# Optimization experiments

Hardware: AMD Instinct MI355X
Metric: run time of the kernel (lower is better)

Reference implementation:

```python
import jax, jax.numpy as jnp
import numpy as np

EMBED_DIM = 1024
N_HEADS = 16
HEAD_DIM = EMBED_DIM // N_HEADS


def setup_inputs() -> dict:
    key = jax.random.key(0)
    k_x, k_wi, k_bi, k_wo, k_bo = jax.random.split(key, 5)
    B, N, C = 4, 2048, EMBED_DIM
    scale = 1.0 / np.sqrt(C)
    return {
        "x": jax.random.normal(k_x, (B, N, C), dtype=jnp.float32),
        "w_in": jax.random.normal(k_wi, (C, 3 * C), dtype=jnp.float32) * scale,
        "b_in": jax.random.normal(k_bi, (3 * C,), dtype=jnp.float32) * 0.01,
        "w_out": jax.random.normal(k_wo, (C, C), dtype=jnp.float32) * scale,
        "b_out": jax.random.normal(k_bo, (C,), dtype=jnp.float32) * 0.01,
    }


def reference(x, w_in, b_in, w_out, b_out):
    B, N, C = x.shape
    H, D = N_HEADS, HEAD_DIM
    qkv = x @ w_in + b_in  # (B, N, 3C)
    q, k, v = jnp.split(qkv, 3, axis=-1)
    # (B, H, N, D)
    q = q.reshape(B, N, H, D).transpose(0, 2, 1, 3)
    k = k.reshape(B, N, H, D).transpose(0, 2, 1, 3)
    v = v.reshape(B, N, H, D).transpose(0, 2, 1, 3)
    # Naive attention: full (B,H,N,N) scores, NO sqrt(d) scaling (as in source)
    scores = jnp.einsum("bhnd,bhmd->bhnm", q, k)
    attn = jax.nn.softmax(scores, axis=-1)
    out = jnp.einsum("bhnm,bhmd->bhnd", attn, v)
    out = out.transpose(0, 2, 1, 3).reshape(B, N, C)
    return out @ w_out + b_out
```

## Files before the change

kernel.cpp:

```cpp
#include <hip/hip_runtime.h>
#include <hip/hip_bf16.h>
#include <stdint.h>

typedef __attribute__((ext_vector_type(8))) __bf16 bf8v;
typedef __attribute__((ext_vector_type(4))) float f4v;

#define L2E 1.44269504088896f

__device__ __forceinline__ unsigned short f2bf(float f) {
  union { float f; unsigned u; } v; v.f = f;
  unsigned r = v.u + 0x7fffu + ((v.u >> 16) & 1u);
  return (unsigned short)(r >> 16);
}

__device__ __forceinline__ unsigned pk2bf(float f0, float f1) {
  union { __hip_bfloat162 h; unsigned u; } c;
  c.h = __float22bfloat162_rn(make_float2(f0, f1));
  return c.u;
}

__device__ __forceinline__ float exp2_hw(float x) {
  return __builtin_amdgcn_exp2f(x);
}

__device__ __forceinline__ void gl_lds16(const void* g, void* l) {
  __builtin_amdgcn_global_load_lds(
      (__attribute__((address_space(1))) void*)(g),
      (__attribute__((address_space(3))) void*)(l), 16, 0, 0);
}

__device__ __forceinline__ void store_out(unsigned short* p, float v) { *p = f2bf(v); }
__device__ __forceinline__ void store_out(float* p, float v) { *p = v; }

__global__ void prep_kernel(const float* __restrict__ x,
                            const float* __restrict__ w_in,
                            const float* __restrict__ w_out,
                            unsigned short* __restrict__ xb,
                            unsigned short* __restrict__ wiT,
                            unsigned short* __restrict__ woT) {
  __shared__ float tile[32][33];
  int bx = blockIdx.x;
  if (bx < 8192) {
    int i = bx * 256 + threadIdx.x;
    float4 v = ((const float4*)x)[i];
    ushort4 o;
    o.x = f2bf(v.x); o.y = f2bf(v.y); o.z = f2bf(v.z); o.w = f2bf(v.w);
    ((ushort4*)xb)[i] = o;
    return;
  }
  int idx = bx - 8192;
  int bxx = idx & 127, byy = idx >> 7;
  const float* in; unsigned short* out; int C, c0;
  if (bxx < 96) { in = w_in;  out = wiT; C = 3072; c0 = bxx * 32; }
  else          { in = w_out; out = woT; C = 1024; c0 = (bxx - 96) * 32; }
  int r0 = byy * 32;
  int tx = threadIdx.x & 31, ty = threadIdx.x >> 5;
#pragma unroll
  for (int j = 0; j < 4; ++j)
    tile[ty + 8 * j][tx] = in[(size_t)(r0 + ty + 8 * j) * C + c0 + tx];
  __syncthreads();
#pragma unroll
  for (int j = 0; j < 4; ++j)
    out[(size_t)(c0 + ty + 8 * j) * 1024 + r0 + tx] = f2bf(tile[tx][ty + 8 * j]);
}

__global__ void transpose_v_kernel(const unsigned short* __restrict__ qkv,
                                   unsigned short* __restrict__ vtg) {
  __shared__ unsigned short tile[32][33];
  int bh = blockIdx.z;
  int d0 = blockIdx.y * 32;
  int n0 = blockIdx.x * 32;
  int b = bh >> 4, h = bh & 15;
  int tx = threadIdx.x, ty = threadIdx.y;
  const unsigned short* src = qkv + (size_t)b * 2048 * 3072 + 2048 + h * 64 + d0;
#pragma unroll
  for (int j = 0; j < 4; ++j)
    tile[ty + 8 * j][tx] = src[(size_t)(n0 + ty + 8 * j) * 3072 + tx];
  __syncthreads();
  unsigned short* dst = vtg + ((size_t)bh * 64) * 2048;
#pragma unroll
  for (int j = 0; j < 4; ++j)
    dst[(size_t)(d0 + ty + 8 * j) * 2048 + n0 + tx] = tile[tx][ty + 8 * j];
}

template <typename OutT, bool SCALE>
__global__ __launch_bounds__(512, 2) void gemm256(
    const unsigned short* __restrict__ A,
    const unsigned short* __restrict__ BT,
    const float* __restrict__ bias,
    OutT* __restrict__ C,
    int N, int K, int nbx, int scale_ncols, float scale) {
  __shared__ __align__(16) unsigned short As[2][256 * 64];
  __shared__ __align__(16) unsigned short Bs[2][128 * 64];
  const int tid = threadIdx.x;
  const int wave = tid >> 6, lane = tid & 63;
  const int lo = lane & 15, hi = lane >> 4;
  const int wm = wave >> 1, wn = wave & 1;

  const int cpx = gridDim.x >> 3;
  const int s = (blockIdx.x & 7) * cpx + (blockIdx.x >> 3);
  const int by = s / nbx, bx = s - by * nbx;
  const int m0 = by * 256, n0 = bx * 128;

  const int srow = lane >> 3;
  const int scol = (((lane & 7) ^ (srow & 7)) * 8);
  const unsigned short* gA = A + (size_t)(m0 + wave * 8 + srow) * K + scol;
  const unsigned short* gB = BT + (size_t)(n0 + wave * 8 + srow) * K + scol;

  const int csw0 = ((hi ^ (lo & 7)) * 8);
  const int csw1 = (((4 + hi) ^ (lo & 7)) * 8);
  const int rA = wm * 64;
  const int rB = wn * 64;

  f4v acc[4][4] = {};
  const int nt = K >> 6;

#pragma unroll
  for (int j = 0; j < 4; ++j)
    gl_lds16(gA + (size_t)(j * 64) * K, &As[0][(j * 64 + wave * 8) * 64]);
#pragma unroll
  for (int j = 0; j < 2; ++j)
    gl_lds16(gB + (size_t)(j * 64) * K, &Bs[0][(j * 64 + wave * 8) * 64]);

  for (int t = 0; t < nt; ++t) {
    const int c = t & 1;
    __builtin_amdgcn_s_barrier();
    __builtin_amdgcn_sched_barrier(0);
    if (t + 1 < nt) {
      const unsigned short* gA1 = gA + (size_t)(t + 1) * 64;
      const unsigned short* gB1 = gB + (size_t)(t + 1) * 64;
#pragma unroll
      for (int j = 0; j < 4; ++j)
        gl_lds16(gA1 + (size_t)(j * 64) * K, &As[c ^ 1][(j * 64 + wave * 8) * 64]);
#pragma unroll
      for (int j = 0; j < 2; ++j)
        gl_lds16(gB1 + (size_t)(j * 64) * K, &Bs[c ^ 1][(j * 64 + wave * 8) * 64]);
      asm volatile("s_waitcnt vmcnt(6)" ::: "memory");
    } else {
      asm volatile("s_waitcnt vmcnt(0)" ::: "memory");
    }
    __builtin_amdgcn_sched_barrier(0);
    __builtin_amdgcn_s_barrier();
    __builtin_amdgcn_sched_barrier(0);

    bf8v b[4][2];
#pragma unroll
    for (int fn = 0; fn < 4; ++fn) {
      b[fn][0] = *(const bf8v*)&Bs[c][(rB + fn * 16 + lo) * 64 + csw0];
      b[fn][1] = *(const bf8v*)&Bs[c][(rB + fn * 16 + lo) * 64 + csw1];
    }
#pragma unroll
    for (int p = 0; p < 2; ++p) {
      bf8v a[2][2];
#pragma unroll
      for (int i = 0; i < 2; ++i) {
        a[i][0] = *(const bf8v*)&As[c][(rA + (p * 2 + i) * 16 + lo) * 64 + csw0];
        a[i][1] = *(const bf8v*)&As[c][(rA + (p * 2 + i) * 16 + lo) * 64 + csw1];
      }
      __builtin_amdgcn_s_setprio(1);
#pragma unroll
      for (int ks = 0; ks < 2; ++ks)
#pragma unroll
        for (int i = 0; i < 2; ++i)
#pragma unroll
          for (int fn = 0; fn < 4; ++fn)
            acc[p * 2 + i][fn] = __builtin_amdgcn_mfma_f32_16x16x32_bf16(
                a[i][ks], b[fn][ks], acc[p * 2 + i][fn], 0, 0, 0);
      __builtin_amdgcn_s_setprio(0);
    }
  }

#pragma unroll
  for (int i = 0; i < 4; ++i) {
#pragma unroll
    for (int r = 0; r < 4; ++r) {
      int row = m0 + wm * 64 + i * 16 + hi * 4 + r;
#pragma unroll
      for (int j = 0; j < 4; ++j) {
        int col = n0 + wn * 64 + j * 16 + lo;
        float v = acc[i][j][r] + bias[col];
        if (SCALE && col < scale_ncols) v *= scale;
        store_out(&C[(size_t)row * N + col], v);
      }
    }
  }
}

#define FSTR 72

__global__ __launch_bounds__(256, 2) void flash_attn(
    const unsigned short* __restrict__ qkv,
    const unsigned short* __restrict__ vtg,
    unsigned short* __restrict__ y) {
  __shared__ __align__(16) unsigned short Ps[256 * FSTR];
  __shared__ __align__(16) unsigned short Kt[2][64 * FSTR];
  __shared__ __align__(16) unsigned short Vt[2][64 * FSTR];
  const int tid = threadIdx.x;
  const int wave = tid >> 6, lane = tid & 63;
  const int lo = lane & 15, hi = lane >> 4;

  const int lin = blockIdx.x;
  const int swz = (lin & 7) * 64 + (lin >> 3);
  const int q0 = (swz & 7) << 8;
  const int h  = (swz >> 3) & 15;
  const int b  = swz >> 7;

  const size_t base = (size_t)b * 2048 * 3072;
  const int qoff = h * 64, koff = 1024 + h * 64;
  const unsigned short* vsrc = vtg + (size_t)(b * 16 + h) * 64 * 2048;

  const int m_st = tid >> 3, c_st = tid & 7;
  const unsigned short* kg = qkv + base + koff;
  float4 rk0, rk1, rv0, rv1;
  auto kv_load = [&](int kt) {
    const int mb = kt * 64;
    rk0 = *(const float4*)(kg + (size_t)(mb + m_st) * 3072 + c_st * 8);
    rk1 = *(const float4*)(kg + (size_t)(mb + m_st + 32) * 3072 + c_st * 8);
    rv0 = *(const float4*)(vsrc + (size_t)m_st * 2048 + mb + c_st * 8);
    rv1 = *(const float4*)(vsrc + (size_t)(m_st + 32) * 2048 + mb + c_st * 8);
  };
  auto kv_write = [&](int buf) {
    *(float4*)&Kt[buf][m_st * FSTR + c_st * 8] = rk0;
    *(float4*)&Kt[buf][(m_st + 32) * FSTR + c_st * 8] = rk1;
    *(float4*)&Vt[buf][m_st * FSTR + c_st * 8] = rv0;
    *(float4*)&Vt[buf][(m_st + 32) * FSTR + c_st * 8] = rv1;
  };

  kv_load(0);

#pragma unroll
  for (int i = 0; i < 8; ++i) {
    int cid = i * 256 + tid;
    int m = cid >> 3, c = cid & 7;
    *(float4*)&Ps[m * FSTR + c * 8] =
        *(const float4*)(qkv + base + (size_t)(q0 + m) * 3072 + qoff + c * 8);
  }
  __syncthreads();
  bf8v bq[4][2];
#pragma unroll
  for (int qt = 0; qt < 4; ++qt)
#pragma unroll
    for (int ks = 0; ks < 2; ++ks)
      bq[qt][ks] = *(const bf8v*)&Ps[(wave * 64 + qt * 16 + lo) * FSTR + ks * 32 + hi * 8];

  f4v O[4][4] = {};
  f4v acc_l[4] = {};
  union { bf8v v; unsigned short u[8]; } onesu;
#pragma unroll
  for (int i = 0; i < 8; ++i) onesu.u[i] = 0x3F80;
  const bf8v ones = onesu.v;

  kv_write(0);
  kv_load(1);
  asm volatile("s_waitcnt lgkmcnt(0)" ::: "memory");
  __builtin_amdgcn_s_barrier();
  asm volatile("" ::: "memory");

  for (int kt = 0; kt < 32; ++kt) {
    const int c = kt & 1;
    if (kt < 31) {
      kv_write(c ^ 1);
      if (kt < 30) kv_load(kt + 2);
    }

#pragma unroll
    for (int ct = 0; ct < 4; ++ct) {
      f4v s[4] = {{}, {}, {}, {}};
      __builtin_amdgcn_s_setprio(1);
#pragma unroll
      for (int ks = 0; ks < 2; ++ks) {
        bf8v ak = *(const bf8v*)&Kt[c][(ct * 16 + lo) * FSTR + ks * 32 + hi * 8];
#pragma unroll
        for (int qt = 0; qt < 4; ++qt)
          s[qt] = __builtin_amdgcn_mfma_f32_16x16x32_bf16(ak, bq[qt][ks], s[qt], 0, 0, 0);
      }
      __builtin_amdgcn_s_setprio(0);
#pragma unroll
      for (int qt = 0; qt < 4; ++qt) {
        float p0 = exp2_hw(s[qt][0]), p1 = exp2_hw(s[qt][1]);
        float p2 = exp2_hw(s[qt][2]), p3 = exp2_hw(s[qt][3]);
        uint2 w; w.x = pk2bf(p0, p1); w.y = pk2bf(p2, p3);
        *(uint2*)&Ps[(wave * 64 + qt * 16 + lo) * FSTR + ct * 16 + hi * 4] = w;
      }
    }

#pragma unroll
    for (int ks = 0; ks < 2; ++ks) {
      bf8v ap[4];
#pragma unroll
      for (int qt = 0; qt < 4; ++qt)
        ap[qt] = *(const bf8v*)&Ps[(wave * 64 + qt * 16 + lo) * FSTR + ks * 32 + hi * 8];
      __builtin_amdgcn_s_setprio(1);
#pragma unroll
      for (int qt = 0; qt < 4; ++qt)
        acc_l[qt] = __builtin_amdgcn_mfma_f32_16x16x32_bf16(ap[qt], ones, acc_l[qt], 0, 0, 0);
#pragma unroll
      for (int dt = 0; dt < 4; ++dt) {
        bf8v bv = *(const bf8v*)&Vt[c][(dt * 16 + lo) * FSTR + ks * 32 + hi * 8];
#pragma unroll
        for (int qt = 0; qt < 4; ++qt)
          O[qt][dt] = __builtin_amdgcn_mfma_f32_16x16x32_bf16(ap[qt], bv, O[qt][dt], 0, 0, 0);
      }
      __builtin_amdgcn_s_setprio(0);
    }

    asm volatile("s_waitcnt lgkmcnt(0)" ::: "memory");
    __builtin_amdgcn_s_barrier();
    asm volatile("" ::: "memory");
  }

#pragma unroll
  for (int qt = 0; qt < 4; ++qt) {
#pragma unroll
    for (int r = 0; r < 4; ++r) {
      float inv = 1.f / acc_l[qt][r];
      int row = q0 + wave * 64 + qt * 16 + hi * 4 + r;
      size_t orow = ((size_t)b * 2048 + row) * 1024 + h * 64;
#pragma unroll
      for (int dt = 0; dt < 4; ++dt)
        y[orow + dt * 16 + lo] = f2bf(O[qt][dt][r] * inv);
    }
  }
}

extern "C" void kernel_launch(void* const* d_in, const int* in_sizes, int n_in,
                              void* d_out, int out_size, void* d_ws, size_t ws_size,
                              hipStream_t stream) {
  (void)in_sizes; (void)n_in; (void)out_size; (void)ws_size;
  const float* x     = (const float*)d_in[0];
  const float* w_in  = (const float*)d_in[1];
  const float* b_in  = (const float*)d_in[2];
  const float* w_out = (const float*)d_in[3];
  const float* b_out = (const float*)d_in[4];

  unsigned short* xb  = (unsigned short*)d_ws;
  unsigned short* wiT = xb  + (size_t)8192 * 1024;
  unsigned short* woT = wiT + (size_t)3072 * 1024;
  unsigned short* qkv = woT + (size_t)1024 * 1024;
  unsigned short* yb  = qkv + (size_t)8192 * 3072;
  unsigned short* vtg = xb;

  prep_kernel<<<12288, 256, 0, stream>>>(x, w_in, w_out, xb, wiT, woT);

  gemm256<unsigned short, true><<<768, 512, 0, stream>>>(
      xb, wiT, b_in, qkv, 3072, 1024, 24, 1024, L2E);
  transpose_v_kernel<<<dim3(64, 2, 64), dim3(32, 8), 0, stream>>>(qkv, vtg);
  flash_attn<<<512, 256, 0, stream>>>(qkv, vtg, yb);
  gemm256<float, false><<<256, 512, 0, stream>>>(
      yb, woT, b_out, (float*)d_out, 1024, 1024, 8, 0, 1.0f);
}
```

Before: 278.6 us.

## Load K/V fragments directly from global memory, drop LDS staging and barriers

The flash attention kernel now has each wave read its K and V MFMA operand fragments straight from global memory into registers, instead of staging them cooperatively through double-buffered shared-memory tiles. Q fragments are also read directly. This removes the LDS K/V buffers and the per-iteration block barrier, so waves can run independently. In exchange, every wave redundantly fetches the full K/V tile (four times more global/L2 traffic), and the loads are no longer prefetched ahead, so memory latency is exposed inside the loop.

```diff
diff --git a/kernel.cpp b/kernel.cpp
--- a/kernel.cpp
+++ b/kernel.cpp
@@ -193,8 +193,6 @@
     const unsigned short* __restrict__ vtg,
     unsigned short* __restrict__ y) {
   __shared__ __align__(16) unsigned short Ps[256 * FSTR];
-  __shared__ __align__(16) unsigned short Kt[2][64 * FSTR];
-  __shared__ __align__(16) unsigned short Vt[2][64 * FSTR];
   const int tid = threadIdx.x;
   const int wave = tid >> 6, lane = tid & 63;
   const int lo = lane & 15, hi = lane >> 4;
@@ -208,40 +206,15 @@
   const size_t base = (size_t)b * 2048 * 3072;
   const int qoff = h * 64, koff = 1024 + h * 64;
   const unsigned short* vsrc = vtg + (size_t)(b * 16 + h) * 64 * 2048;
-
-  const int m_st = tid >> 3, c_st = tid & 7;
   const unsigned short* kg = qkv + base + koff;
-  float4 rk0, rk1, rv0, rv1;
-  auto kv_load = [&](int kt) {
-    const int mb = kt * 64;
-    rk0 = *(const float4*)(kg + (size_t)(mb + m_st) * 3072 + c_st * 8);
-    rk1 = *(const float4*)(kg + (size_t)(mb + m_st + 32) * 3072 + c_st * 8);
-    rv0 = *(const float4*)(vsrc + (size_t)m_st * 2048 + mb + c_st * 8);
-    rv1 = *(const float4*)(vsrc + (size_t)(m_st + 32) * 2048 + mb + c_st * 8);
-  };
-  auto kv_write = [&](int buf) {
-    *(float4*)&Kt[buf][m_st * FSTR + c_st * 8] = rk0;
-    *(float4*)&Kt[buf][(m_st + 32) * FSTR + c_st * 8] = rk1;
-    *(float4*)&Vt[buf][m_st * FSTR + c_st * 8] = rv0;
-    *(float4*)&Vt[buf][(m_st + 32) * FSTR + c_st * 8] = rv1;
-  };
-
-  kv_load(0);
-
-#pragma unroll
-  for (int i = 0; i < 8; ++i) {
-    int cid = i * 256 + tid;
-    int m = cid >> 3, c = cid & 7;
-    *(float4*)&Ps[m * FSTR + c * 8] =
-        *(const float4*)(qkv + base + (size_t)(q0 + m) * 3072 + qoff + c * 8);
-  }
-  __syncthreads();
+
   bf8v bq[4][2];
 #pragma unroll
   for (int qt = 0; qt < 4; ++qt)
 #pragma unroll
     for (int ks = 0; ks < 2; ++ks)
-      bq[qt][ks] = *(const bf8v*)&Ps[(wave * 64 + qt * 16 + lo) * FSTR + ks * 32 + hi * 8];
+      bq[qt][ks] = *(const bf8v*)(qkv + base +
+          (size_t)(q0 + wave * 64 + qt * 16 + lo) * 3072 + qoff + ks * 32 + hi * 8);
 
   f4v O[4][4] = {};
   f4v acc_l[4] = {};
@@ -250,37 +223,41 @@
   for (int i = 0; i < 8; ++i) onesu.u[i] = 0x3F80;
   const bf8v ones = onesu.v;
 
-  kv_write(0);
-  kv_load(1);
-  asm volatile("s_waitcnt lgkmcnt(0)" ::: "memory");
-  __builtin_amdgcn_s_barrier();
-  asm volatile("" ::: "memory");
+  const int prow = (wave * 64 + lo) * FSTR;
 
   for (int kt = 0; kt < 32; ++kt) {
-    const int c = kt & 1;
-    if (kt < 31) {
-      kv_write(c ^ 1);
-      if (kt < 30) kv_load(kt + 2);
-    }
+    const unsigned short* kb = kg + (size_t)kt * 64 * 3072;
+    const unsigned short* vb = vsrc + kt * 64;
+
+    bf8v kn[4][2];
+#pragma unroll
+    for (int ct = 0; ct < 4; ++ct)
+#pragma unroll
+      for (int ks = 0; ks < 2; ++ks)
+        kn[ct][ks] = *(const bf8v*)(kb + (size_t)(ct * 16 + lo) * 3072 + ks * 32 + hi * 8);
+    bf8v vn[4][2];
+#pragma unroll
+    for (int dt = 0; dt < 4; ++dt)
+#pragma unroll
+      for (int ks = 0; ks < 2; ++ks)
+        vn[dt][ks] = *(const bf8v*)(vb + (size_t)(dt * 16 + lo) * 2048 + ks * 32 + hi * 8);
 
 #pragma unroll
     for (int ct = 0; ct < 4; ++ct) {
       f4v s[4] = {{}, {}, {}, {}};
       __builtin_amdgcn_s_setprio(1);
 #pragma unroll
-      for (int ks = 0; ks < 2; ++ks) {
-        bf8v ak = *(const bf8v*)&Kt[c][(ct * 16 + lo) * FSTR + ks * 32 + hi * 8];
+      for (int ks = 0; ks < 2; ++ks)
 #pragma unroll
         for (int qt = 0; qt < 4; ++qt)
-          s[qt] = __builtin_amdgcn_mfma_f32_16x16x32_bf16(ak, bq[qt][ks], s[qt], 0, 0, 0);
-      }
+          s[qt] = __builtin_amdgcn_mfma_f32_16x16x32_bf16(kn[ct][ks], bq[qt][ks], s[qt], 0, 0, 0);
       __builtin_amdgcn_s_setprio(0);
 #pragma unroll
       for (int qt = 0; qt < 4; ++qt) {
         float p0 = exp2_hw(s[qt][0]), p1 = exp2_hw(s[qt][1]);
         float p2 = exp2_hw(s[qt][2]), p3 = exp2_hw(s[qt][3]);
         uint2 w; w.x = pk2bf(p0, p1); w.y = pk2bf(p2, p3);
-        *(uint2*)&Ps[(wave * 64 + qt * 16 + lo) * FSTR + ct * 16 + hi * 4] = w;
+        *(uint2*)&Ps[prow + qt * 16 * FSTR + ct * 16 + hi * 4] = w;
       }
     }
 
@@ -289,24 +266,18 @@
       bf8v ap[4];
 #pragma unroll
       for (int qt = 0; qt < 4; ++qt)
-        ap[qt] = *(const bf8v*)&Ps[(wave * 64 + qt * 16 + lo) * FSTR + ks * 32 + hi * 8];
+        ap[qt] = *(const bf8v*)&Ps[prow + qt * 16 * FSTR + ks * 32 + hi * 8];
       __builtin_amdgcn_s_setprio(1);
 #pragma unroll
       for (int qt = 0; qt < 4; ++qt)
         acc_l[qt] = __builtin_amdgcn_mfma_f32_16x16x32_bf16(ap[qt], ones, acc_l[qt], 0, 0, 0);
 #pragma unroll
-      for (int dt = 0; dt < 4; ++dt) {
-        bf8v bv = *(const bf8v*)&Vt[c][(dt * 16 + lo) * FSTR + ks * 32 + hi * 8];
+      for (int dt = 0; dt < 4; ++dt)
 #pragma unroll
         for (int qt = 0; qt < 4; ++qt)
-          O[qt][dt] = __builtin_amdgcn_mfma_f32_16x16x32_bf16(ap[qt], bv, O[qt][dt], 0, 0, 0);
-      }
+          O[qt][dt] = __builtin_amdgcn_mfma_f32_16x16x32_bf16(ap[qt], vn[dt][ks], O[qt][dt], 0, 0, 0);
       __builtin_amdgcn_s_setprio(0);
     }
-
-    asm volatile("s_waitcnt lgkmcnt(0)" ::: "memory");
-    __builtin_amdgcn_s_barrier();
-    asm volatile("" ::: "memory");
   }
 
 #pragma unroll
```

After: 322.8 us. +15.9%, slower.

## Fuse V transpose into QKV GEMM epilogue and drop transpose kernel

Applied to the files above, without the earlier changes.

The QKV projection GEMM epilogue now writes Q and K into a compact 2048-wide buffer and writes V directly in transposed per-head layout, packing four consecutive tokens into one 8-byte store. This removes the separate transpose_v kernel launch and its extra read and write of V through global memory. Flash attention is updated to the new Q/K row stride. The V stores are strided across rows of the transposed layout, so that part of the epilogue may coalesce less well than before.

```diff
diff --git a/kernel.cpp b/kernel.cpp
--- a/kernel.cpp
+++ b/kernel.cpp
@@ -28,9 +28,6 @@
       (__attribute__((address_space(1))) void*)(g),
       (__attribute__((address_space(3))) void*)(l), 16, 0, 0);
 }
-
-__device__ __forceinline__ void store_out(unsigned short* p, float v) { *p = f2bf(v); }
-__device__ __forceinline__ void store_out(float* p, float v) { *p = v; }
 
 __global__ void prep_kernel(const float* __restrict__ x,
                             const float* __restrict__ w_in,
@@ -64,32 +61,14 @@
     out[(size_t)(c0 + ty + 8 * j) * 1024 + r0 + tx] = f2bf(tile[tx][ty + 8 * j]);
 }
 
-__global__ void transpose_v_kernel(const unsigned short* __restrict__ qkv,
-                                   unsigned short* __restrict__ vtg) {
-  __shared__ unsigned short tile[32][33];
-  int bh = blockIdx.z;
-  int d0 = blockIdx.y * 32;
-  int n0 = blockIdx.x * 32;
-  int b = bh >> 4, h = bh & 15;
-  int tx = threadIdx.x, ty = threadIdx.y;
-  const unsigned short* src = qkv + (size_t)b * 2048 * 3072 + 2048 + h * 64 + d0;
-#pragma unroll
-  for (int j = 0; j < 4; ++j)
-    tile[ty + 8 * j][tx] = src[(size_t)(n0 + ty + 8 * j) * 3072 + tx];
-  __syncthreads();
-  unsigned short* dst = vtg + ((size_t)bh * 64) * 2048;
-#pragma unroll
-  for (int j = 0; j < 4; ++j)
-    dst[(size_t)(d0 + ty + 8 * j) * 2048 + n0 + tx] = tile[tx][ty + 8 * j];
-}
-
-template <typename OutT, bool SCALE>
+template <int MODE>
 __global__ __launch_bounds__(512, 2) void gemm256(
     const unsigned short* __restrict__ A,
     const unsigned short* __restrict__ BT,
     const float* __restrict__ bias,
-    OutT* __restrict__ C,
-    int N, int K, int nbx, int scale_ncols, float scale) {
+    void* __restrict__ Cv,
+    unsigned short* __restrict__ vtg,
+    int N, int K, int nbx, float scale) {
   __shared__ __align__(16) unsigned short As[2][256 * 64];
   __shared__ __align__(16) unsigned short Bs[2][128 * 64];
   const int tid = threadIdx.x;
@@ -173,14 +152,32 @@
 #pragma unroll
   for (int i = 0; i < 4; ++i) {
 #pragma unroll
-    for (int r = 0; r < 4; ++r) {
-      int row = m0 + wm * 64 + i * 16 + hi * 4 + r;
-#pragma unroll
-      for (int j = 0; j < 4; ++j) {
-        int col = n0 + wn * 64 + j * 16 + lo;
-        float v = acc[i][j][r] + bias[col];
-        if (SCALE && col < scale_ncols) v *= scale;
-        store_out(&C[(size_t)row * N + col], v);
+    for (int j = 0; j < 4; ++j) {
+      const int col = n0 + wn * 64 + j * 16 + lo;
+      const int row0 = m0 + wm * 64 + i * 16 + hi * 4;
+      if (MODE == 0) {
+        float* C = (float*)Cv;
+#pragma unroll
+        for (int r = 0; r < 4; ++r)
+          C[(size_t)(row0 + r) * N + col] = acc[i][j][r] + bias[col];
+      } else {
+        unsigned short* C = (unsigned short*)Cv;
+        const float bb = bias[col];
+        if (col < 2048) {
+          const float sc = (col < 1024) ? scale : 1.0f;
+#pragma unroll
+          for (int r = 0; r < 4; ++r)
+            C[(size_t)(row0 + r) * 2048 + col] = f2bf((acc[i][j][r] + bb) * sc);
+        } else {
+          const int d = (col - 2048) & 63, hh = (col - 2048) >> 6;
+          const int bbt = row0 >> 11, tok = row0 & 2047;
+          ushort4 o;
+          o.x = f2bf(acc[i][j][0] + bb);
+          o.y = f2bf(acc[i][j][1] + bb);
+          o.z = f2bf(acc[i][j][2] + bb);
+          o.w = f2bf(acc[i][j][3] + bb);
+          *(ushort4*)&vtg[((((size_t)bbt * 16 + hh) * 64 + d) * 2048) + tok] = o;
+        }
       }
     }
   }
@@ -189,7 +186,7 @@
 #define FSTR 72
 
 __global__ __launch_bounds__(256, 2) void flash_attn(
-    const unsigned short* __restrict__ qkv,
+    const unsigned short* __restrict__ qk,
     const unsigned short* __restrict__ vtg,
     unsigned short* __restrict__ y) {
   __shared__ __align__(16) unsigned short Ps[256 * FSTR];
@@ -205,17 +202,17 @@
   const int h  = (swz >> 3) & 15;
   const int b  = swz >> 7;
 
-  const size_t base = (size_t)b * 2048 * 3072;
+  const size_t base = (size_t)b * 2048 * 2048;
   const int qoff = h * 64, koff = 1024 + h * 64;
   const unsigned short* vsrc = vtg + (size_t)(b * 16 + h) * 64 * 2048;
 
   const int m_st = tid >> 3, c_st = tid & 7;
-  const unsigned short* kg = qkv + base + koff;
+  const unsigned short* kg = qk + base + koff;
   float4 rk0, rk1, rv0, rv1;
   auto kv_load = [&](int kt) {
     const int mb = kt * 64;
-    rk0 = *(const float4*)(kg + (size_t)(mb + m_st) * 3072 + c_st * 8);
-    rk1 = *(const float4*)(kg + (size_t)(mb + m_st + 32) * 3072 + c_st * 8);
+    rk0 = *(const float4*)(kg + (size_t)(mb + m_st) * 2048 + c_st * 8);
+    rk1 = *(const float4*)(kg + (size_t)(mb + m_st + 32) * 2048 + c_st * 8);
     rv0 = *(const float4*)(vsrc + (size_t)m_st * 2048 + mb + c_st * 8);
     rv1 = *(const float4*)(vsrc + (size_t)(m_st + 32) * 2048 + mb + c_st * 8);
   };
@@ -233,7 +230,7 @@
     int cid = i * 256 + tid;
     int m = cid >> 3, c = cid & 7;
     *(float4*)&Ps[m * FSTR + c * 8] =
-        *(const float4*)(qkv + base + (size_t)(q0 + m) * 3072 + qoff + c * 8);
+        *(const float4*)(qk + base + (size_t)(q0 + m) * 2048 + qoff + c * 8);
   }
   __syncthreads();
   bf8v bq[4][2];
@@ -336,16 +333,13 @@
   unsigned short* xb  = (unsigned short*)d_ws;
   unsigned short* wiT = xb  + (size_t)8192 * 1024;
   unsigned short* woT = wiT + (size_t)3072 * 1024;
-  unsigned short* qkv = woT + (size_t)1024 * 1024;
-  unsigned short* yb  = qkv + (size_t)8192 * 3072;
-  unsigned short* vtg = xb;
+  unsigned short* qk  = woT + (size_t)1024 * 1024;
+  unsigned short* vtg = qk  + (size_t)8192 * 2048;
+  unsigned short* yb  = vtg + (size_t)64 * 64 * 2048;
 
   prep_kernel<<<12288, 256, 0, stream>>>(x, w_in, w_out, xb, wiT, woT);
 
-  gemm256<unsigned short, true><<<768, 512, 0, stream>>>(
-      xb, wiT, b_in, qkv, 3072, 1024, 24, 1024, L2E);
-  transpose_v_kernel<<<dim3(64, 2, 64), dim3(32, 8), 0, stream>>>(qkv, vtg);
-  flash_attn<<<512, 256, 0, stream>>>(qkv, vtg, yb);
-  gemm256<float, false><<<256, 512, 0, stream>>>(
-      yb, woT, b_out, (float*)d_out, 1024, 1024, 8, 0, 1.0f);
-}
+  gemm256<1><<<768, 512, 0, stream>>>(xb, wiT, b_in, qk, vtg, 3072, 1024, 24, L2E);
+  flash_attn<<<512, 256, 0, stream>>>(qk, vtg, yb);
+  gemm256<0><<<256, 512, 0, stream>>>(yb, woT, b_out, d_out, nullptr, 1024, 1024, 8, 1.0f);
+}
```

After: 274.8 us. No clear change (-1.4%).
